# Optimization experiments

Measured on AMD Instinct MI355X. Metric: run time of the kernel, lower is better.

## Reference

```python
import jax, jax.numpy as jnp
import numpy as np

ALPHA_LIM = (float(np.exp(-1.0 / 5.0)), float(np.exp(-1.0 / 25.0)))
BETA_LIM = (float(np.exp(-1.0 / 30.0)), float(np.exp(-1.0 / 120.0)))
A_LIM = (-1.0, 1.0)
B_LIM = (0.0, 2.0)
THRESHOLD = 1.0


@jax.custom_vjp
def spike_boxcar(x):
    # Heaviside forward, boxcar surrogate gradient
    return (x > 0).astype(x.dtype)


def _spike_fwd(x):
    return spike_boxcar(x), x


def _spike_bwd(x, g):
    return (jnp.where(jnp.abs(x) <= 0.5, g, jnp.zeros_like(g)),)


spike_boxcar.defvjp(_spike_fwd, _spike_bwd)


def setup_inputs() -> dict:
    key = jax.random.key(0)
    ks = jax.random.split(key, 9)
    B, T, I, H = 128, 512, 512, 512
    return {
        "x": jax.random.normal(ks[0], (B, T, I), dtype=jnp.float32),
        "W": jax.random.normal(ks[1], (H, I), dtype=jnp.float32) / np.sqrt(I),
        "alpha": jax.random.uniform(ks[2], (H,), dtype=jnp.float32),
        "beta": jax.random.uniform(ks[3], (H,), dtype=jnp.float32),
        "a": jax.random.uniform(ks[4], (H,), dtype=jnp.float32),
        "b": jax.random.uniform(ks[5], (H,), dtype=jnp.float32),
        "u0": jax.random.uniform(ks[6], (B, H), dtype=jnp.float32),
        "w0": jax.random.uniform(ks[7], (B, H), dtype=jnp.float32),
        "s0": jax.random.uniform(ks[8], (B, H), dtype=jnp.float32),
    }


def reference(x, W, alpha, beta, a, b, u0, w0, s0):
    # x: [B, T, I]; W: [H, I] (nn.Linear weight, no bias)
    alpha = jnp.clip(alpha, ALPHA_LIM[0], ALPHA_LIM[1])
    beta = jnp.clip(beta, BETA_LIM[0], BETA_LIM[1])
    a = jnp.clip(a, A_LIM[0], A_LIM[1])
    b = jnp.clip(b, B_LIM[0], B_LIM[1])

    Wx = jnp.einsum("bti,hi->bth", x, W)  # [B, T, H]
    Wx_t = jnp.transpose(Wx, (1, 0, 2))    # [T, B, H] for scan over time

    def step(carry, wx_t):
        ut, wt, st = carry
        wt = beta * wt + a * ut + b * st
        ut = alpha * (ut - st) + (1.0 - alpha) * (wx_t - wt)
        st = spike_boxcar(ut - THRESHOLD)
        return (ut, wt, st), st

    _, s = jax.lax.scan(step, (u0, w0, s0), Wx_t)  # s: [T, B, H]
    return jnp.transpose(s, (1, 0, 2))  # [B, T, H]
```

## Files before the change

kernel.cpp:

```cpp
#include <hip/hip_runtime.h>
#include <hip/hip_bf16.h>


#define M_SZ 65536
#define H_SZ 512
#define K_SZ 512
#define B_SZ 128
#define T_SZ 512
#define LSTR 132

typedef __attribute__((ext_vector_type(4))) float f32x4;

__device__ __forceinline__ bool detect_bf16(const unsigned int* __restrict__ w) {
  int c = 0;
#pragma unroll
  for (int i = 0; i < 64; ++i) {
    unsigned int e = (w[i] >> 7) & 0xffu;
    c += (e >= 115u && e <= 131u) ? 1 : 0;
  }
  return c > 32;
}

template <bool ISB>
__device__ __forceinline__ f32x4 ld4t(const void* __restrict__ p, size_t off) {
  if constexpr (!ISB) {
    return *reinterpret_cast<const f32x4*>(reinterpret_cast<const float*>(p) + off);
  } else {
    uint2 v = *reinterpret_cast<const uint2*>(reinterpret_cast<const unsigned short*>(p) + off);
    f32x4 r;
    r.x = __uint_as_float((v.x & 0xffffu) << 16);
    r.y = __uint_as_float(v.x & 0xffff0000u);
    r.z = __uint_as_float((v.y & 0xffffu) << 16);
    r.w = __uint_as_float(v.y & 0xffff0000u);
    return r;
  }
}

template <bool ISB>
__device__ __forceinline__ float ld1t(const void* __restrict__ p, int i) {
  if constexpr (!ISB) return reinterpret_cast<const float*>(p)[i];
  return __uint_as_float((unsigned int)(reinterpret_cast<const unsigned short*>(p)[i]) << 16);
}

template <bool ISB>
__device__ __forceinline__ void gemm_body(const void* __restrict__ X,
                                          const void* __restrict__ Wm,
                                          float* __restrict__ C,
                                          float* __restrict__ As,
                                          float* __restrict__ Bs) {
  const int tid = threadIdx.x;
  const int r0 = tid >> 2;
  const int q0 = (tid & 3) * 4;
  const int tx = tid & 15;
  const int ty = tid >> 4;
  const size_t M0 = (size_t)(blockIdx.x >> 2) * 128;
  const int N0 = (blockIdx.x & 3) * 128;

  float acc[8][8];
#pragma unroll
  for (int i = 0; i < 8; ++i)
#pragma unroll
    for (int j = 0; j < 8; ++j) acc[i][j] = 0.0f;

  const size_t aoff0 = (M0 + r0) * K_SZ + q0;
  const size_t aoff1 = (M0 + r0 + 64) * K_SZ + q0;
  const size_t boff0 = (size_t)(N0 + r0) * K_SZ + q0;
  const size_t boff1 = (size_t)(N0 + r0 + 64) * K_SZ + q0;

  f32x4 pa0 = ld4t<ISB>(X, aoff0), pa1 = ld4t<ISB>(X, aoff1);
  f32x4 pb0 = ld4t<ISB>(Wm, boff0), pb1 = ld4t<ISB>(Wm, boff1);

  for (int kk = 0; kk < K_SZ; kk += 16) {
    __syncthreads();
    As[(q0 + 0) * LSTR + r0] = pa0.x; As[(q0 + 1) * LSTR + r0] = pa0.y;
    As[(q0 + 2) * LSTR + r0] = pa0.z; As[(q0 + 3) * LSTR + r0] = pa0.w;
    As[(q0 + 0) * LSTR + r0 + 64] = pa1.x; As[(q0 + 1) * LSTR + r0 + 64] = pa1.y;
    As[(q0 + 2) * LSTR + r0 + 64] = pa1.z; As[(q0 + 3) * LSTR + r0 + 64] = pa1.w;
    Bs[(q0 + 0) * LSTR + r0] = pb0.x; Bs[(q0 + 1) * LSTR + r0] = pb0.y;
    Bs[(q0 + 2) * LSTR + r0] = pb0.z; Bs[(q0 + 3) * LSTR + r0] = pb0.w;
    Bs[(q0 + 0) * LSTR + r0 + 64] = pb1.x; Bs[(q0 + 1) * LSTR + r0 + 64] = pb1.y;
    Bs[(q0 + 2) * LSTR + r0 + 64] = pb1.z; Bs[(q0 + 3) * LSTR + r0 + 64] = pb1.w;
    __syncthreads();
    if (kk + 16 < K_SZ) {
      pa0 = ld4t<ISB>(X, aoff0 + kk + 16); pa1 = ld4t<ISB>(X, aoff1 + kk + 16);
      pb0 = ld4t<ISB>(Wm, boff0 + kk + 16); pb1 = ld4t<ISB>(Wm, boff1 + kk + 16);
    }
#pragma unroll
    for (int k = 0; k < 16; ++k) {
      const f32x4 a0 = *reinterpret_cast<const f32x4*>(As + k * LSTR + ty * 4);
      const f32x4 a1 = *reinterpret_cast<const f32x4*>(As + k * LSTR + 64 + ty * 4);
      const f32x4 b0 = *reinterpret_cast<const f32x4*>(Bs + k * LSTR + tx * 4);
      const f32x4 b1 = *reinterpret_cast<const f32x4*>(Bs + k * LSTR + 64 + tx * 4);
      const float av[8] = {a0.x, a0.y, a0.z, a0.w, a1.x, a1.y, a1.z, a1.w};
      const float bv[8] = {b0.x, b0.y, b0.z, b0.w, b1.x, b1.y, b1.z, b1.w};
#pragma unroll
      for (int i = 0; i < 8; ++i)
#pragma unroll
        for (int j = 0; j < 8; ++j) acc[i][j] += av[i] * bv[j];
    }
  }

#pragma unroll
  for (int r = 0; r < 8; ++r) {
    const size_t m = M0 + ((r < 4) ? (ty * 4 + r) : (64 + ty * 4 + (r - 4)));
    float* Cp = C + m * H_SZ + N0;
    f32x4 v0 = {acc[r][0], acc[r][1], acc[r][2], acc[r][3]};
    f32x4 v1 = {acc[r][4], acc[r][5], acc[r][6], acc[r][7]};
    __builtin_nontemporal_store(v0, reinterpret_cast<f32x4*>(Cp + tx * 4));
    __builtin_nontemporal_store(v1, reinterpret_cast<f32x4*>(Cp + 64 + tx * 4));
  }
}

__global__ __launch_bounds__(256) void sgemm_bt(const void* __restrict__ X,
                                                const void* __restrict__ Wm,
                                                float* __restrict__ C) {
  __shared__ float As[16 * LSTR];
  __shared__ float Bs[16 * LSTR];
  if (detect_bf16(reinterpret_cast<const unsigned int*>(X)))
    gemm_body<true>(X, Wm, C, As, Bs);
  else
    gemm_body<false>(X, Wm, C, As, Bs);
}

#define SCT 8
#define SNC (T_SZ / SCT)

template <bool ISB>
__device__ __forceinline__ void scan_body(
    const float* __restrict__ wx, const void* __restrict__ alpha_p,
    const void* __restrict__ beta_p, const void* __restrict__ a_p,
    const void* __restrict__ b_p, const void* __restrict__ u0p,
    const void* __restrict__ w0p, const void* __restrict__ s0p,
    void* __restrict__ out) {
  const int lane = threadIdx.x;
  const int b = blockIdx.x >> 3;
  const int h0 = (blockIdx.x & 7) * 64;
  const int h = h0 + lane;

  const float al = fminf(fmaxf(ld1t<ISB>(alpha_p, h), (float)0.8187307530779818),
                         (float)0.9607894391523232);
  const float be = fminf(fmaxf(ld1t<ISB>(beta_p, h), (float)0.9672161004820059),
                         (float)0.9917013044213351);
  const float av = fminf(fmaxf(ld1t<ISB>(a_p, h), -1.0f), 1.0f);
  const float bv = fminf(fmaxf(ld1t<ISB>(b_p, h), 0.0f), 2.0f);
  const float om = __fsub_rn(1.0f, al);

  const int bh = b * H_SZ + h;
  float u = ld1t<ISB>(u0p, bh);
  float w = ld1t<ISB>(w0p, bh);
  float s = ld1t<ISB>(s0p, bh);

  const float* xb = wx + (size_t)b * T_SZ * H_SZ + h;
  float* outf = reinterpret_cast<float*>(out);
  __hip_bfloat16* outb = reinterpret_cast<__hip_bfloat16*>(out);
  const size_t ob0 = (size_t)b * T_SZ * H_SZ + h;

  float ring[4][SCT];
  auto loadc = [&](float* dst, int c) {
#pragma unroll
    for (int j = 0; j < SCT; ++j) {
      int t = c * SCT + j;
      t = (t < T_SZ) ? t : (T_SZ - 1);
      dst[j] = xb[(size_t)t * H_SZ];
    }
  };

  loadc(ring[0], 0); loadc(ring[1], 1); loadc(ring[2], 2); loadc(ring[3], 3);

  for (int c0 = 0; c0 < SNC; c0 += 4) {
#pragma unroll
    for (int p = 0; p < 4; ++p) {
      const int c = c0 + p;
#pragma unroll
      for (int j = 0; j < SCT; ++j) {
        const float cur = ring[p][j];
        w = __fadd_rn(__fadd_rn(__fmul_rn(be, w), __fmul_rn(av, u)), __fmul_rn(bv, s));
        u = __fadd_rn(__fmul_rn(al, __fsub_rn(u, s)), __fmul_rn(om, __fsub_rn(cur, w)));
        s = (u > 1.0f) ? 1.0f : 0.0f;
        const size_t o = ob0 + (size_t)(c * SCT + j) * H_SZ;
        if constexpr (ISB) outb[o] = __float2bfloat16(s);
        else outf[o] = s;
      }
      loadc(ring[p], c + 4);
    }
  }
}

__global__ __launch_bounds__(64) void lif_scan(
    const float* __restrict__ wx, const void* __restrict__ X,
    const void* __restrict__ alpha_p, const void* __restrict__ beta_p,
    const void* __restrict__ a_p, const void* __restrict__ b_p,
    const void* __restrict__ u0p, const void* __restrict__ w0p,
    const void* __restrict__ s0p, void* __restrict__ out) {
  if (detect_bf16(reinterpret_cast<const unsigned int*>(X)))
    scan_body<true>(wx, alpha_p, beta_p, a_p, b_p, u0p, w0p, s0p, out);
  else
    scan_body<false>(wx, alpha_p, beta_p, a_p, b_p, u0p, w0p, s0p, out);
}

extern "C" void kernel_launch(void* const* d_in, const int* in_sizes, int n_in,
                              void* d_out, int out_size, void* d_ws, size_t ws_size,
                              hipStream_t stream) {
  const void* X = d_in[0];
  const void* Wm = d_in[1];
  float* ws = reinterpret_cast<float*>(d_ws);

  sgemm_bt<<<dim3((M_SZ / 128) * (H_SZ / 128)), dim3(256), 0, stream>>>(X, Wm, ws);

  lif_scan<<<dim3(B_SZ * 8), dim3(64), 0, stream>>>(
      ws, X, d_in[2], d_in[3], d_in[4], d_in[5], d_in[6], d_in[7], d_in[8], d_out);
}
```

Measured before the change: 622.2 us.

## Fuse input projection GEMM and adaptive LIF scan into one kernel

```diff
diff --git a/kernel.cpp b/kernel.cpp
--- a/kernel.cpp
+++ b/kernel.cpp
@@ -43,170 +43,156 @@
 }
 
 template <bool ISB>
-__device__ __forceinline__ void gemm_body(const void* __restrict__ X,
-                                          const void* __restrict__ Wm,
-                                          float* __restrict__ C,
-                                          float* __restrict__ As,
-                                          float* __restrict__ Bs) {
+__device__ __forceinline__ void fused_body(
+    const void* __restrict__ X, const void* __restrict__ Wm,
+    const void* __restrict__ alpha_p, const void* __restrict__ beta_p,
+    const void* __restrict__ a_p, const void* __restrict__ b_p,
+    const void* __restrict__ u0p, const void* __restrict__ w0p,
+    const void* __restrict__ s0p, void* __restrict__ out,
+    float* __restrict__ As, float* __restrict__ Bs, float* __restrict__ st) {
   const int tid = threadIdx.x;
   const int r0 = tid >> 2;
   const int q0 = (tid & 3) * 4;
   const int tx = tid & 15;
   const int ty = tid >> 4;
-  const size_t M0 = (size_t)(blockIdx.x >> 2) * 128;
+  const int b = blockIdx.x >> 2;
   const int N0 = (blockIdx.x & 3) * 128;
 
-  float acc[8][8];
-#pragma unroll
-  for (int i = 0; i < 8; ++i)
-#pragma unroll
-    for (int j = 0; j < 8; ++j) acc[i][j] = 0.0f;
+  float* su = st;        float* sw = st + 128;  float* ss = st + 256;
+  float* pal = st + 384; float* pbe = st + 512; float* pav = st + 640;
+  float* pbv = st + 768; float* pom = st + 896;
 
-  const size_t aoff0 = (M0 + r0) * K_SZ + q0;
-  const size_t aoff1 = (M0 + r0 + 64) * K_SZ + q0;
-  const size_t boff0 = (size_t)(N0 + r0) * K_SZ + q0;
-  const size_t boff1 = (size_t)(N0 + r0 + 64) * K_SZ + q0;
-
-  f32x4 pa0 = ld4t<ISB>(X, aoff0), pa1 = ld4t<ISB>(X, aoff1);
-  f32x4 pb0 = ld4t<ISB>(Wm, boff0), pb1 = ld4t<ISB>(Wm, boff1);
-
-  for (int kk = 0; kk < K_SZ; kk += 16) {
-    __syncthreads();
-    As[(q0 + 0) * LSTR + r0] = pa0.x; As[(q0 + 1) * LSTR + r0] = pa0.y;
-    As[(q0 + 2) * LSTR + r0] = pa0.z; As[(q0 + 3) * LSTR + r0] = pa0.w;
-    As[(q0 + 0) * LSTR + r0 + 64] = pa1.x; As[(q0 + 1) * LSTR + r0 + 64] = pa1.y;
-    As[(q0 + 2) * LSTR + r0 + 64] = pa1.z; As[(q0 + 3) * LSTR + r0 + 64] = pa1.w;
-    Bs[(q0 + 0) * LSTR + r0] = pb0.x; Bs[(q0 + 1) * LSTR + r0] = pb0.y;
-    Bs[(q0 + 2) * LSTR + r0] = pb0.z; Bs[(q0 + 3) * LSTR + r0] = pb0.w;
-    Bs[(q0 + 0) * LSTR + r0 + 64] = pb1.x; Bs[(q0 + 1) * LSTR + r0 + 64] = pb1.y;
-    Bs[(q0 + 2) * LSTR + r0 + 64] = pb1.z; Bs[(q0 + 3) * LSTR + r0 + 64] = pb1.w;
-    __syncthreads();
-    if (kk + 16 < K_SZ) {
-      pa0 = ld4t<ISB>(X, aoff0 + kk + 16); pa1 = ld4t<ISB>(X, aoff1 + kk + 16);
-      pb0 = ld4t<ISB>(Wm, boff0 + kk + 16); pb1 = ld4t<ISB>(Wm, boff1 + kk + 16);
-    }
-#pragma unroll
-    for (int k = 0; k < 16; ++k) {
-      const f32x4 a0 = *reinterpret_cast<const f32x4*>(As + k * LSTR + ty * 4);
-      const f32x4 a1 = *reinterpret_cast<const f32x4*>(As + k * LSTR + 64 + ty * 4);
-      const f32x4 b0 = *reinterpret_cast<const f32x4*>(Bs + k * LSTR + tx * 4);
-      const f32x4 b1 = *reinterpret_cast<const f32x4*>(Bs + k * LSTR + 64 + tx * 4);
-      const float av[8] = {a0.x, a0.y, a0.z, a0.w, a1.x, a1.y, a1.z, a1.w};
-      const float bv[8] = {b0.x, b0.y, b0.z, b0.w, b1.x, b1.y, b1.z, b1.w};
-#pragma unroll
-      for (int i = 0; i < 8; ++i)
-#pragma unroll
-        for (int j = 0; j < 8; ++j) acc[i][j] += av[i] * bv[j];
-    }
+  if (tid < 128) {
+    const int h = N0 + tid;
+    const float al = fminf(fmaxf(ld1t<ISB>(alpha_p, h), (float)0.8187307530779818),
+                           (float)0.9607894391523232);
+    const float be = fminf(fmaxf(ld1t<ISB>(beta_p, h), (float)0.9672161004820059),
+                           (float)0.9917013044213351);
+    pal[tid] = al;
+    pbe[tid] = be;
+    pav[tid] = fminf(fmaxf(ld1t<ISB>(a_p, h), -1.0f), 1.0f);
+    pbv[tid] = fminf(fmaxf(ld1t<ISB>(b_p, h), 0.0f), 2.0f);
+    pom[tid] = __fsub_rn(1.0f, al);
+    const int bh = b * H_SZ + h;
+    su[tid] = ld1t<ISB>(u0p, bh);
+    sw[tid] = ld1t<ISB>(w0p, bh);
+    ss[tid] = ld1t<ISB>(s0p, bh);
   }
 
+  float* outf = reinterpret_cast<float*>(out);
+  unsigned int* outu = reinterpret_cast<unsigned int*>(out);
+
+  for (int tt = 0; tt < 4; ++tt) {
+    const size_t M0 = (size_t)b * T_SZ + tt * 128;
+
+    float acc[8][8];
 #pragma unroll
-  for (int r = 0; r < 8; ++r) {
-    const size_t m = M0 + ((r < 4) ? (ty * 4 + r) : (64 + ty * 4 + (r - 4)));
-    float* Cp = C + m * H_SZ + N0;
-    f32x4 v0 = {acc[r][0], acc[r][1], acc[r][2], acc[r][3]};
-    f32x4 v1 = {acc[r][4], acc[r][5], acc[r][6], acc[r][7]};
-    __builtin_nontemporal_store(v0, reinterpret_cast<f32x4*>(Cp + tx * 4));
-    __builtin_nontemporal_store(v1, reinterpret_cast<f32x4*>(Cp + 64 + tx * 4));
-  }
-}
+    for (int i = 0; i < 8; ++i)
+#pragma unroll
+      for (int j = 0; j < 8; ++j) acc[i][j] = 0.0f;
 
-__global__ __launch_bounds__(256) void sgemm_bt(const void* __restrict__ X,
-                                                const void* __restrict__ Wm,
-                                                float* __restrict__ C) {
-  __shared__ float As[16 * LSTR];
-  __shared__ float Bs[16 * LSTR];
-  if (detect_bf16(reinterpret_cast<const unsigned int*>(X)))
-    gemm_body<true>(X, Wm, C, As, Bs);
-  else
-    gemm_body<false>(X, Wm, C, As, Bs);
-}
+    const size_t aoff0 = (M0 + r0) * K_SZ + q0;
+    const size_t aoff1 = (M0 + r0 + 64) * K_SZ + q0;
+    const size_t boff0 = (size_t)(N0 + r0) * K_SZ + q0;
+    const size_t boff1 = (size_t)(N0 + r0 + 64) * K_SZ + q0;
 
-#define SCT 8
-#define SNC (T_SZ / SCT)
+    f32x4 pa0 = ld4t<ISB>(X, aoff0), pa1 = ld4t<ISB>(X, aoff1);
+    f32x4 pb0 = ld4t<ISB>(Wm, boff0), pb1 = ld4t<ISB>(Wm, boff1);
 
-template <bool ISB>
-__device__ __forceinline__ void scan_body(
-    const float* __restrict__ wx, const void* __restrict__ alpha_p,
-    const void* __restrict__ beta_p, const void* __restrict__ a_p,
-    const void* __restrict__ b_p, const void* __restrict__ u0p,
-    const void* __restrict__ w0p, const void* __restrict__ s0p,
-    void* __restrict__ out) {
-  const int lane = threadIdx.x;
-  const int b = blockIdx.x >> 3;
-  const int h0 = (blockIdx.x & 7) * 64;
-  const int h = h0 + lane;
+    for (int kk = 0; kk < K_SZ; kk += 16) {
+      __syncthreads();
+      As[(q0 + 0) * LSTR + r0] = pa0.x; As[(q0 + 1) * LSTR + r0] = pa0.y;
+      As[(q0 + 2) * LSTR + r0] = pa0.z; As[(q0 + 3) * LSTR + r0] = pa0.w;
+      As[(q0 + 0) * LSTR + r0 + 64] = pa1.x; As[(q0 + 1) * LSTR + r0 + 64] = pa1.y;
+      As[(q0 + 2) * LSTR + r0 + 64] = pa1.z; As[(q0 + 3) * LSTR + r0 + 64] = pa1.w;
+      Bs[(q0 + 0) * LSTR + r0] = pb0.x; Bs[(q0 + 1) * LSTR + r0] = pb0.y;
+      Bs[(q0 + 2) * LSTR + r0] = pb0.z; Bs[(q0 + 3) * LSTR + r0] = pb0.w;
+      Bs[(q0 + 0) * LSTR + r0 + 64] = pb1.x; Bs[(q0 + 1) * LSTR + r0 + 64] = pb1.y;
+      Bs[(q0 + 2) * LSTR + r0 + 64] = pb1.z; Bs[(q0 + 3) * LSTR + r0 + 64] = pb1.w;
+      __syncthreads();
+      if (kk + 16 < K_SZ) {
+        pa0 = ld4t<ISB>(X, aoff0 + kk + 16); pa1 = ld4t<ISB>(X, aoff1 + kk + 16);
+        pb0 = ld4t<ISB>(Wm, boff0 + kk + 16); pb1 = ld4t<ISB>(Wm, boff1 + kk + 16);
+      }
+#pragma unroll
+      for (int k = 0; k < 16; ++k) {
+        const f32x4 a0 = *reinterpret_cast<const f32x4*>(As + k * LSTR + ty * 4);
+        const f32x4 a1 = *reinterpret_cast<const f32x4*>(As + k * LSTR + 64 + ty * 4);
+        const f32x4 b0 = *reinterpret_cast<const f32x4*>(Bs + k * LSTR + tx * 4);
+        const f32x4 b1 = *reinterpret_cast<const f32x4*>(Bs + k * LSTR + 64 + tx * 4);
+        const float av[8] = {a0.x, a0.y, a0.z, a0.w, a1.x, a1.y, a1.z, a1.w};
+        const float bv[8] = {b0.x, b0.y, b0.z, b0.w, b1.x, b1.y, b1.z, b1.w};
+#pragma unroll
+        for (int i = 0; i < 8; ++i)
+#pragma unroll
+          for (int j = 0; j < 8; ++j) acc[i][j] += av[i] * bv[j];
+      }
+    }
 
-  const float al = fminf(fmaxf(ld1t<ISB>(alpha_p, h), (float)0.8187307530779818),
-                         (float)0.9607894391523232);
-  const float be = fminf(fmaxf(ld1t<ISB>(beta_p, h), (float)0.9672161004820059),
-                         (float)0.9917013044213351);
-  const float av = fminf(fmaxf(ld1t<ISB>(a_p, h), -1.0f), 1.0f);
-  const float bv = fminf(fmaxf(ld1t<ISB>(b_p, h), 0.0f), 2.0f);
-  const float om = __fsub_rn(1.0f, al);
-
-  const int bh = b * H_SZ + h;
-  float u = ld1t<ISB>(u0p, bh);
-  float w = ld1t<ISB>(w0p, bh);
-  float s = ld1t<ISB>(s0p, bh);
-
-  const float* xb = wx + (size_t)b * T_SZ * H_SZ + h;
-  float* outf = reinterpret_cast<float*>(out);
-  __hip_bfloat16* outb = reinterpret_cast<__hip_bfloat16*>(out);
-  const size_t ob0 = (size_t)b * T_SZ * H_SZ + h;
-
-  float ring[4][SCT];
-  auto loadc = [&](float* dst, int c) {
+    for (int p = 0; p < 32; ++p) {
+      const bool act = (p < 16) ? (ty == p) : (ty == p - 16);
+      if (act) {
+        float spkA[4][4];
+        float spkB[4][4];
 #pragma unroll
-    for (int j = 0; j < SCT; ++j) {
-      int t = c * SCT + j;
-      t = (t < T_SZ) ? t : (T_SZ - 1);
-      dst[j] = xb[(size_t)t * H_SZ];
-    }
-  };
-
-  loadc(ring[0], 0); loadc(ring[1], 1); loadc(ring[2], 2); loadc(ring[3], 3);
-
-  for (int c0 = 0; c0 < SNC; c0 += 4) {
+        for (int jj = 0; jj < 8; ++jj) {
+          const int n = (jj < 4) ? (tx * 4 + jj) : (64 + tx * 4 + (jj - 4));
+          float u = su[n], w = sw[n], s = ss[n];
+          const float al = pal[n], be = pbe[n], av = pav[n], bv = pbv[n], om = pom[n];
 #pragma unroll
-    for (int p = 0; p < 4; ++p) {
-      const int c = c0 + p;
+          for (int rr = 0; rr < 4; ++rr) {
+            const float cur = (p < 16) ? acc[rr][jj] : acc[4 + rr][jj];
+            w = __fadd_rn(__fadd_rn(__fmul_rn(be, w), __fmul_rn(av, u)), __fmul_rn(bv, s));
+            u = __fadd_rn(__fmul_rn(al, __fsub_rn(u, s)), __fmul_rn(om, __fsub_rn(cur, w)));
+            s = (u > 1.0f) ? 1.0f : 0.0f;
+            if (jj < 4) spkA[rr][jj] = s;
+            else spkB[rr][jj - 4] = s;
+          }
+          su[n] = u; sw[n] = w; ss[n] = s;
+        }
 #pragma unroll
-      for (int j = 0; j < SCT; ++j) {
-        const float cur = ring[p][j];
-        w = __fadd_rn(__fadd_rn(__fmul_rn(be, w), __fmul_rn(av, u)), __fmul_rn(bv, s));
-        u = __fadd_rn(__fmul_rn(al, __fsub_rn(u, s)), __fmul_rn(om, __fsub_rn(cur, w)));
-        s = (u > 1.0f) ? 1.0f : 0.0f;
-        const size_t o = ob0 + (size_t)(c * SCT + j) * H_SZ;
-        if constexpr (ISB) outb[o] = __float2bfloat16(s);
-        else outf[o] = s;
+        for (int rr = 0; rr < 4; ++rr) {
+          const size_t trow = ((size_t)b * T_SZ + tt * 128 + 4 * p + rr) * H_SZ + N0;
+          if constexpr (!ISB) {
+            f32x4 v0 = {spkA[rr][0], spkA[rr][1], spkA[rr][2], spkA[rr][3]};
+            f32x4 v1 = {spkB[rr][0], spkB[rr][1], spkB[rr][2], spkB[rr][3]};
+            *reinterpret_cast<f32x4*>(outf + trow + tx * 4) = v0;
+            *reinterpret_cast<f32x4*>(outf + trow + 64 + tx * 4) = v1;
+          } else {
+            uint2 d0, d1;
+            d0.x = (__float_as_uint(spkA[rr][1]) & 0xffff0000u) | (__float_as_uint(spkA[rr][0]) >> 16);
+            d0.y = (__float_as_uint(spkA[rr][3]) & 0xffff0000u) | (__float_as_uint(spkA[rr][2]) >> 16);
+            d1.x = (__float_as_uint(spkB[rr][1]) & 0xffff0000u) | (__float_as_uint(spkB[rr][0]) >> 16);
+            d1.y = (__float_as_uint(spkB[rr][3]) & 0xffff0000u) | (__float_as_uint(spkB[rr][2]) >> 16);
+            *reinterpret_cast<uint2*>(outu + (trow + tx * 4) / 2) = d0;
+            *reinterpret_cast<uint2*>(outu + (trow + 64 + tx * 4) / 2) = d1;
+          }
+        }
       }
-      loadc(ring[p], c + 4);
+      __syncthreads();
     }
   }
 }
 
-__global__ __launch_bounds__(64) void lif_scan(
-    const float* __restrict__ wx, const void* __restrict__ X,
+__global__ __launch_bounds__(256) void adlif_fused(
+    const void* __restrict__ X, const void* __restrict__ Wm,
     const void* __restrict__ alpha_p, const void* __restrict__ beta_p,
     const void* __restrict__ a_p, const void* __restrict__ b_p,
     const void* __restrict__ u0p, const void* __restrict__ w0p,
     const void* __restrict__ s0p, void* __restrict__ out) {
+  __shared__ float As[16 * LSTR];
+  __shared__ float Bs[16 * LSTR];
+  __shared__ float st[8 * 128];
   if (detect_bf16(reinterpret_cast<const unsigned int*>(X)))
-    scan_body<true>(wx, alpha_p, beta_p, a_p, b_p, u0p, w0p, s0p, out);
+    fused_body<true>(X, Wm, alpha_p, beta_p, a_p, b_p, u0p, w0p, s0p, out, As, Bs, st);
   else
-    scan_body<false>(wx, alpha_p, beta_p, a_p, b_p, u0p, w0p, s0p, out);
+    fused_body<false>(X, Wm, alpha_p, beta_p, a_p, b_p, u0p, w0p, s0p, out, As, Bs, st);
 }
 
 extern "C" void kernel_launch(void* const* d_in, const int* in_sizes, int n_in,
                               void* d_out, int out_size, void* d_ws, size_t ws_size,
                               hipStream_t stream) {
-  const void* X = d_in[0];
-  const void* Wm = d_in[1];
-  float* ws = reinterpret_cast<float*>(d_ws);
-
-  sgemm_bt<<<dim3((M_SZ / 128) * (H_SZ / 128)), dim3(256), 0, stream>>>(X, Wm, ws);
-
-  lif_scan<<<dim3(B_SZ * 8), dim3(64), 0, stream>>>(
-      ws, X, d_in[2], d_in[3], d_in[4], d_in[5], d_in[6], d_in[7], d_in[8], d_out);
+  adlif_fused<<<dim3(B_SZ * 4), dim3(256), 0, stream>>>(
+      d_in[0], d_in[1], d_in[2], d_in[3], d_in[4], d_in[5], d_in[6], d_in[7],
+      d_in[8], d_out);
 }
```

New measurement: 688.8 us. +10.7%, slower.
